# Optimization experiments

Measured on AMD Instinct MI355X. Metric: run time of the kernel, lower is better.

## Reference

```python
import jax, jax.numpy as jnp
import numpy as np
from jax import lax

INPUT_SIZE = 64          # classifier ROI size (init kwarg)
IMG = 640                # source image H=W
PROV, ALPHA, AD = 38, 25, 35
CONF_THRES, IOU_THRES = 0.25, 0.45
MAX_DET = 300            # yolov5 NMS max detections
FLAT = 16 * (INPUT_SIZE // 2) ** 2  # 16384


def setup_inputs() -> dict:
    key = jax.random.key(0)
    ks = jax.random.split(key, 12)
    B, N = 1, 25200
    xy = jax.random.uniform(ks[0], (B, N, 2), minval=32.0, maxval=608.0)
    wh = jax.random.uniform(ks[1], (B, N, 2), minval=16.0, maxval=128.0)
    obj = jax.random.uniform(ks[2], (B, N, 1))
    cls = jax.random.uniform(ks[3], (B, N, 1))
    preds = jnp.concatenate([xy, wh, obj, cls], axis=-1)  # [1,N,6] xywh+obj+cls
    image = jax.random.normal(ks[4], (B, 3, IMG, IMG), dtype=jnp.float32)
    W_conv = 0.1 * jax.random.normal(ks[5], (16, 3, 3, 3), dtype=jnp.float32)
    b_conv = jnp.zeros((16,), jnp.float32)
    W1 = 0.01 * jax.random.normal(ks[6], (8, FLAT, 128), dtype=jnp.float32)
    b1 = jnp.zeros((8, 128), jnp.float32)
    W2p = 0.05 * jax.random.normal(ks[7], (128, PROV), dtype=jnp.float32)
    b2p = jnp.zeros((PROV,), jnp.float32)
    W2a = 0.05 * jax.random.normal(ks[8], (128, ALPHA), dtype=jnp.float32)
    b2a = jnp.zeros((ALPHA,), jnp.float32)
    W2d = 0.05 * jax.random.normal(ks[9], (6, 128, AD), dtype=jnp.float32)
    b2d = jnp.zeros((6, AD), jnp.float32)
    return {"preds": preds, "image": image, "W_conv": W_conv, "b_conv": b_conv,
            "W1": W1, "b1": b1, "W2p": W2p, "b2p": b2p, "W2a": W2a, "b2a": b2a,
            "W2d": W2d, "b2d": b2d}


def _pairwise_iou(b):
    # b: [K,4] xyxy
    x1, y1, x2, y2 = b[:, 0], b[:, 1], b[:, 2], b[:, 3]
    area = (x2 - x1) * (y2 - y1)
    iw = jnp.clip(jnp.minimum(x2[:, None], x2[None, :]) - jnp.maximum(x1[:, None], x1[None, :]), 0.0)
    ih = jnp.clip(jnp.minimum(y2[:, None], y2[None, :]) - jnp.maximum(y1[:, None], y1[None, :]), 0.0)
    inter = iw * ih
    return inter / (area[:, None] + area[None, :] - inter + 1e-7)


def reference(preds, image, W_conv, b_conv, W1, b1, W2p, b2p, W2a, b2a, W2d, b2d):
    # ---- NMS (yolov5-style, single class) ----
    p = preds[0]                                   # [N,6]
    score = p[:, 4] * p[:, 5]                      # obj_conf * cls_conf
    xy, wh = p[:, 0:2], p[:, 2:4]
    boxes = jnp.concatenate([xy - wh / 2, xy + wh / 2], axis=-1)  # xyxy
    masked = jnp.where(score > CONF_THRES, score, -jnp.inf)
    top_s, idx = lax.top_k(masked, MAX_DET)        # sorted desc
    b = boxes[idx]                                 # [K,4]
    valid = top_s > CONF_THRES
    ious = _pairwise_iou(b)                        # [K,K]
    ar = jnp.arange(MAX_DET)

    def body(i, keep):
        sup = jnp.any((ious[i] > IOU_THRES) & keep & (ar < i))
        return keep.at[i].set(keep[i] & jnp.logical_not(sup))

    keep = lax.fori_loop(0, MAX_DET, body, valid)  # greedy suppression

    # ---- fixed-size ROI crop at box top-left (clipped) ----
    x1 = jnp.clip(jnp.round(b[:, 0]).astype(jnp.int32), 0, IMG - INPUT_SIZE)
    y1 = jnp.clip(jnp.round(b[:, 1]).astype(jnp.int32), 0, IMG - INPUT_SIZE)
    img0 = image[0]                                # [3,H,W]
    crops = jax.vmap(lambda y, x: lax.dynamic_slice(img0, (0, y, x), (3, INPUT_SIZE, INPUT_SIZE)))(y1, x1)

    # ---- LicensePlateClassifier: conv->relu->maxpool->flatten->8 heads ----
    conv = lax.conv_general_dilated(crops, W_conv, (1, 1), 'SAME',
                                    dimension_numbers=('NCHW', 'OIHW', 'NCHW'))
    conv = jax.nn.relu(conv + b_conv[None, :, None, None])
    pooled = lax.reduce_window(conv, -jnp.inf, lax.max, (1, 1, 2, 2), (1, 1, 2, 2), 'VALID')
    feats = pooled.reshape(MAX_DET, FLAT)          # NCHW flatten == torch.flatten(x,1)
    h = jax.nn.relu(jnp.einsum('kf,hfd->hkd', feats, W1) + b1[:, None, :])  # [8,K,128]
    out_p = h[0] @ W2p + b2p                       # [K,38]
    out_a = h[1] @ W2a + b2a                       # [K,25]
    out_d = jnp.einsum('hkd,hdo->hko', h[2:], W2d) + b2d[:, None, :]        # [6,K,35]
    out_d = out_d.transpose(1, 0, 2).reshape(MAX_DET, 6 * AD)
    logits = jnp.concatenate([out_p, out_a, out_d], axis=1)  # [K,273]
    return logits * keep.astype(logits.dtype)[:, None]
```

## Files before the change

kernel.cpp:

```cpp
#include <hip/hip_runtime.h>

#define N_PRED 25200
#define CONF 0.25f
#define IOU_THR 0.45f
#define MAXD 300
#define IMGW 640
#define CROPW 64
#define HISTN 16640
#define KSPLIT 16

typedef float f32x4 __attribute__((ext_vector_type(4)));
typedef short s16x8 __attribute__((ext_vector_type(8)));
typedef unsigned long long u64;

#define OFF_HIST   0u
#define OFF_CNT    66560u
#define OFF_CAND   66816u
#define CTRL_BYTES 75008u
#define OFF_BOXES  75008u
#define OFF_XY1    79872u
#define OFF_VALID  82432u
#define OFF_KEEP   83712u
#define OFF_SUP    84992u
#define OFF_FEATS  1325824u
#define OFF_PART   11811584u

__device__ inline unsigned short f2bf(float x) {
  unsigned u = __float_as_uint(x);
  u += 0x7FFFu + ((u >> 16) & 1u);
  return (unsigned short)(u >> 16);
}

__global__ __launch_bounds__(256) void k_hist(const float* __restrict__ preds,
                                              unsigned* __restrict__ hist) {
  int i = blockIdx.x * 256 + threadIdx.x;
  if (i >= N_PRED) return;
  float s = preds[i * 6 + 4] * preds[i * 6 + 5];
  if (s > CONF) atomicAdd(&hist[__float_as_uint(s) >> 16], 1u);
}

__global__ __launch_bounds__(256) void k_compact(const float* __restrict__ preds,
                                                 const unsigned* __restrict__ hist,
                                                 unsigned* __restrict__ cnt,
                                                 u64* __restrict__ cand) {
  __shared__ unsigned s[256];
  __shared__ unsigned scut;
  int t = threadIdx.x;
  int base = t * 65;
  unsigned local = 0;
  for (int i = 0; i < 65; ++i) local += hist[base + i];
  s[t] = local;
  __syncthreads();
  for (int off = 1; off < 256; off <<= 1) {
    unsigned add = (t + off < 256) ? s[t + off] : 0u;
    __syncthreads();
    s[t] += add;
    __syncthreads();
  }
  unsigned incl = s[t];
  unsigned excl = (t < 255) ? s[t + 1] : 0u;
  if (t == 0) scut = 0u;
  __syncthreads();
  if (incl >= (unsigned)MAXD && excl < (unsigned)MAXD) {
    unsigned acc = excl, res = 0u;
    #pragma unroll
    for (int ii = 64; ii >= 0; --ii) {
      acc += hist[base + ii];
      if (res == 0u && acc >= (unsigned)MAXD) res = (unsigned)(base + ii);
    }
    scut = res;
  }
  __syncthreads();
  unsigned cutv = scut;

  int i = blockIdx.x * 256 + t;
  if (i >= N_PRED) return;
  float sc = preds[i * 6 + 4] * preds[i * 6 + 5];
  if (sc <= CONF) return;
  unsigned bits = __float_as_uint(sc);
  if ((bits >> 16) < cutv) return;
  unsigned pos = atomicAdd(cnt, 1u);
  if (pos < 1024u)
    cand[pos] = ((u64)bits << 32) | (u64)(0xFFFFFFFFu - (unsigned)i);
}

__global__ __launch_bounds__(1024) void k_sortprep(const float* __restrict__ preds,
                                                   const u64* __restrict__ cand,
                                                   float* __restrict__ boxes,
                                                   int* __restrict__ xy1,
                                                   float* __restrict__ validf) {
  __shared__ u64 sk[1024];
  int t = threadIdx.x;
  sk[t] = cand[t];
  __syncthreads();
  for (int k = 2; k <= 1024; k <<= 1)
    for (int j = k >> 1; j > 0; j >>= 1) {
      int p = t ^ j;
      if (p > t) {
        u64 a = sk[t], b = sk[p];
        bool up = ((t & k) == 0);
        bool sw = up ? (a < b) : (a > b);
        if (sw) { sk[t] = b; sk[p] = a; }
      }
      __syncthreads();
    }
  if (t < MAXD) {
    u64 key = sk[t];
    if (key != 0ull) {
      int idx = (int)(0xFFFFFFFFu - (unsigned)(key & 0xFFFFFFFFull));
      float cx = preds[idx * 6 + 0], cy = preds[idx * 6 + 1];
      float w  = preds[idx * 6 + 2], h  = preds[idx * 6 + 3];
      float x1 = cx - w * 0.5f, y1 = cy - h * 0.5f;
      float x2 = cx + w * 0.5f, y2 = cy + h * 0.5f;
      boxes[t * 4 + 0] = x1; boxes[t * 4 + 1] = y1;
      boxes[t * 4 + 2] = x2; boxes[t * 4 + 3] = y2;
      int xi = (int)rintf(x1); xi = min(max(xi, 0), IMGW - CROPW);
      int yi = (int)rintf(y1); yi = min(max(yi, 0), IMGW - CROPW);
      xy1[t * 2 + 0] = xi; xy1[t * 2 + 1] = yi;
      validf[t] = 1.0f;
    } else {
      boxes[t * 4 + 0] = 0.f; boxes[t * 4 + 1] = 0.f;
      boxes[t * 4 + 2] = 0.f; boxes[t * 4 + 3] = 0.f;
      xy1[t * 2 + 0] = 0; xy1[t * 2 + 1] = 0;
      validf[t] = 0.f;
    }
  }
}

__global__ __launch_bounds__(320) void k_iou(const float* __restrict__ boxes,
                                             u64* __restrict__ sup) {
  int i = blockIdx.x, t = threadIdx.x;
  int w = t >> 6, lane = t & 63;
  f32x4 bi = *(const f32x4*)&boxes[i * 4];
  f32x4 bj = (t < MAXD) ? *(const f32x4*)&boxes[t * 4]
                        : (f32x4){0.f, 0.f, 0.f, 0.f};
  float ar  = (bi[2] - bi[0]) * (bi[3] - bi[1]);
  float arj = (bj[2] - bj[0]) * (bj[3] - bj[1]);
  float iw = fmaxf(fminf(bi[2], bj[2]) - fmaxf(bi[0], bj[0]), 0.f);
  float ih = fmaxf(fminf(bi[3], bj[3]) - fmaxf(bi[1], bj[1]), 0.f);
  float inter = iw * ih;
  float iou = inter / (ar + arj - inter + 1e-7f);
  u64 bm = __ballot((t < MAXD) && (iou > IOU_THR));
  if (lane == 0) sup[i * 5 + w] = bm;
}

__global__ __launch_bounds__(64) void k_nms(const u64* __restrict__ sup,
                                            const float* __restrict__ validf,
                                            float* __restrict__ keepf) {
  int lane = threadIdx.x;
  u64 srow[5][5];
  #pragma unroll
  for (int c = 0; c < 5; ++c)
    #pragma unroll
    for (int ww = 0; ww < 5; ++ww) srow[c][ww] = 0ull;
  #pragma unroll
  for (int c = 0; c < 5; ++c) {
    int i = c * 64 + lane;
    if (i < MAXD) {
      #pragma unroll
      for (int ww = 0; ww <= c; ++ww) srow[c][ww] = sup[i * 5 + ww];
    }
  }
  u64 validm[5];
  #pragma unroll
  for (int c = 0; c < 5; ++c) {
    int i = c * 64 + lane;
    float vf = (i < MAXD) ? validf[i] : 0.f;
    validm[c] = __ballot(vf > 0.5f);
  }
  u64 kw0 = 0, kw1 = 0, kw2 = 0, kw3 = 0;
  #pragma unroll
  for (int c = 0; c < 5; ++c) {
    bool ext = ((srow[c][0] & kw0) | (srow[c][1] & kw1) |
                (srow[c][2] & kw2) | (srow[c][3] & kw3)) != 0ull;
    u64 alive = validm[c] & __ballot(!ext);
    unsigned mlo = (unsigned)srow[c][c], mhi = (unsigned)(srow[c][c] >> 32);
    u64 rem = alive;
    while (rem) {
      int b = (int)__builtin_ctzll(rem);
      u64 gt = (b == 63) ? 0ull : (~0ull << (b + 1));
      u64 mi = ((u64)(unsigned)__builtin_amdgcn_readlane((int)mhi, b) << 32) |
               (u64)(unsigned)__builtin_amdgcn_readlane((int)mlo, b);
      alive &= ~(mi & gt);
      rem = alive & gt;
    }
    int i = c * 64 + lane;
    if (i < MAXD) keepf[i] = ((alive >> lane) & 1ull) ? 1.f : 0.f;
    if (c == 0) kw0 = alive;
    else if (c == 1) kw1 = alive;
    else if (c == 2) kw2 = alive;
    else if (c == 3) kw3 = alive;
  }
}

__global__ __launch_bounds__(256) void k_cropconv(const float* __restrict__ image,
                                                  const float* __restrict__ Wc,
                                                  const float* __restrict__ bc,
                                                  const int* __restrict__ xy1,
                                                  short* __restrict__ feats) {
  __shared__ __align__(16) float crop[3][10][68];
  int det = blockIdx.x, sl = blockIdx.y, tid = threadIdx.x;
  int pr0 = sl * 4;
  int gyBase = pr0 * 2 - 1;
  int ch = tid >> 4, px = tid & 15;

  float w[27];
  #pragma unroll
  for (int i = 0; i < 27; i++) w[i] = Wc[ch * 27 + i];
  float bias = bc[ch];

  int x0 = xy1[det * 2 + 0], y0 = xy1[det * 2 + 1];
  float sv[8];
  #pragma unroll
  for (int i = 0; i < 8; i++) {
    int u = tid + i * 256;
    float v = 0.f;
    if (u < 1920) {
      int row = u >> 6, x = u & 63;
      int c = row / 10, ry = row - c * 10;
      int gy = gyBase + ry;
      if (gy >= 0 && gy < CROPW)
        v = image[(size_t)c * (IMGW * IMGW) + (y0 + gy) * IMGW + x0 + x];
    }
    sv[i] = v;
  }
  if (tid < 120) {
    int row = tid >> 2, e = tid & 3;
    int c = row / 10, ry = row - c * 10;
    crop[c][ry][(e == 0) ? 0 : (64 + e)] = 0.f;
  }
  #pragma unroll
  for (int i = 0; i < 8; i++) {
    int u = tid + i * 256;
    if (u < 1920) {
      int row = u >> 6, x = u & 63;
      int c = row / 10, ry = row - c * 10;
      crop[c][ry][x + 1] = sv[i];
    }
  }
  __syncthreads();
  #pragma unroll
  for (int pr = 0; pr < 4; pr++) {
    float acc0[4] = {0.f, 0.f, 0.f, 0.f};
    float acc1[4] = {0.f, 0.f, 0.f, 0.f};
    #pragma unroll
    for (int c = 0; c < 3; c++) {
      #pragma unroll
      for (int r = 0; r < 4; r++) {
        const float* rp = &crop[c][2 * pr + r][4 * px];
        f32x4 v4 = *(const f32x4*)rp;
        float2 v2 = *(const float2*)(rp + 4);
        float in[6] = {v4[0], v4[1], v4[2], v4[3], v2.x, v2.y};
        if (r <= 2) {
          const float w0 = w[c * 9 + r * 3], w1 = w[c * 9 + r * 3 + 1],
                      w2 = w[c * 9 + r * 3 + 2];
          #pragma unroll
          for (int q = 0; q < 4; q++)
            acc0[q] += in[q] * w0 + in[q + 1] * w1 + in[q + 2] * w2;
        }
        if (r >= 1) {
          const float w0 = w[c * 9 + (r - 1) * 3], w1 = w[c * 9 + (r - 1) * 3 + 1],
                      w2 = w[c * 9 + (r - 1) * 3 + 2];
          #pragma unroll
          for (int q = 0; q < 4; q++)
            acc1[q] += in[q] * w0 + in[q + 1] * w1 + in[q + 2] * w2;
        }
      }
    }
    float m0 = fmaxf(fmaxf(acc0[0], acc0[1]), fmaxf(acc1[0], acc1[1]));
    float m1 = fmaxf(fmaxf(acc0[2], acc0[3]), fmaxf(acc1[2], acc1[3]));
    unsigned lo = f2bf(fmaxf(m0 + bias, 0.f));
    unsigned hi = f2bf(fmaxf(m1 + bias, 0.f));
    *(unsigned*)&feats[(size_t)det * 16384 + ch * 1024 + (pr0 + pr) * 32 + 2 * px] =
        lo | (hi << 16);
  }
}

__global__ __launch_bounds__(512, 2) void k_gemm(const short* __restrict__ feats,
                                                 const float* __restrict__ W1,
                                                 float* __restrict__ part) {
  __shared__ __align__(16) short As[2][320 * 64];
  int tid = threadIdx.x;
  int wid = tid >> 6, lane = tid & 63;
  int wm = wid & 3, wn = wid >> 2;
  int lr = lane & 15, kg = lane >> 4;
  int ks = blockIdx.x, hd = blockIdx.y, dh = blockIdx.z;
  const int f0 = ks * 1024, d0 = dh * 64;
  const float* w1h = W1 + (size_t)hd * 16384 * 128;

  f32x4 acc[5][2];
  #pragma unroll
  for (int i = 0; i < 5; i++)
    #pragma unroll
    for (int j = 0; j < 2; j++) acc[i][j] = (f32x4){0.f, 0.f, 0.f, 0.f};

  s16x8 aR[5];
  #pragma unroll
  for (int i = 0; i < 5; i++) {
    int ch = tid + i * 512, m = ch >> 3, c = ch & 7;
    aR[i] = *(const s16x8*)(feats + (size_t)m * 16384 + f0 + c * 8);
  }
  const float* bp = w1h + (size_t)(f0 + kg * 8) * 128 + d0 + wn * 32 + lr;
  float bF[2][2][8];
  #pragma unroll
  for (int k32 = 0; k32 < 2; k32++)
    #pragma unroll
    for (int nf = 0; nf < 2; nf++)
      #pragma unroll
      for (int j = 0; j < 8; j++)
        bF[k32][nf][j] = bp[(k32 * 32 + j) * 128 + nf * 16];
  #pragma unroll
  for (int i = 0; i < 5; i++) {
    int ch = tid + i * 512, m = ch >> 3, c = ch & 7;
    *(s16x8*)((char*)&As[0][0] + m * 128 + ((c ^ (m & 7)) << 4)) = aR[i];
  }
  __syncthreads();

  for (int t = 0; t < 16; ++t) {
    int cur = t & 1;
    s16x8 bfr[2][2];
    #pragma unroll
    for (int k32 = 0; k32 < 2; k32++)
      #pragma unroll
      for (int nf = 0; nf < 2; nf++)
        #pragma unroll
        for (int j = 0; j < 8; j++)
          bfr[k32][nf][j] = (short)f2bf(bF[k32][nf][j]);
    bool pf = (t + 1) < 16;
    if (pf) {
      int f1 = f0 + (t + 1) * 64;
      #pragma unroll
      for (int i = 0; i < 5; i++) {
        int ch = tid + i * 512, m = ch >> 3, c = ch & 7;
        aR[i] = *(const s16x8*)(feats + (size_t)m * 16384 + f1 + c * 8);
      }
      const float* bp2 = bp + (size_t)(t + 1) * 64 * 128;
      #pragma unroll
      for (int k32 = 0; k32 < 2; k32++)
        #pragma unroll
        for (int nf = 0; nf < 2; nf++)
          #pragma unroll
          for (int j = 0; j < 8; j++)
            bF[k32][nf][j] = bp2[(k32 * 32 + j) * 128 + nf * 16];
    }
    #pragma unroll
    for (int k32 = 0; k32 < 2; ++k32) {
      s16x8 af[5];
      #pragma unroll
      for (int mf = 0; mf < 5; ++mf) {
        int row = wm * 80 + mf * 16 + lr;
        int c = k32 * 4 + kg;
        af[mf] = *(const s16x8*)((const char*)&As[cur][0] + row * 128 + ((c ^ (row & 7)) << 4));
      }
      #pragma unroll
      for (int nf = 0; nf < 2; ++nf)
        #pragma unroll
        for (int mf = 0; mf < 5; ++mf)
          acc[mf][nf] = __builtin_amdgcn_mfma_f32_16x16x32_bf16(af[mf], bfr[k32][nf], acc[mf][nf], 0, 0, 0);
    }
    if (pf) {
      #pragma unroll
      for (int i = 0; i < 5; i++) {
        int ch = tid + i * 512, m = ch >> 3, c = ch & 7;
        *(s16x8*)((char*)&As[cur ^ 1][0] + m * 128 + ((c ^ (m & 7)) << 4)) = aR[i];
      }
      __syncthreads();
    }
  }
  #pragma unroll
  for (int mf = 0; mf < 5; ++mf)
    #pragma unroll
    for (int nf = 0; nf < 2; ++nf)
      #pragma unroll
      for (int r = 0; r < 4; ++r) {
        int m = wm * 80 + mf * 16 + kg * 4 + r;
        int d = d0 + wn * 32 + nf * 16 + lr;
        part[(((size_t)ks * 8 + hd) * 320 + m) * 128 + d] = acc[mf][nf][r];
      }
}

__global__ __launch_bounds__(320) void k_fc2(const float* __restrict__ part,
                                             const float* __restrict__ b1,
                                             const float* __restrict__ keepf,
                                             const float* __restrict__ W2p,
                                             const float* __restrict__ b2p,
                                             const float* __restrict__ W2a,
                                             const float* __restrict__ b2a,
                                             const float* __restrict__ W2d,
                                             const float* __restrict__ b2d,
                                             float* __restrict__ out) {
  int det = blockIdx.x, t = threadIdx.x;
  __shared__ float hl[1024];
  for (int i = t; i < 1024; i += 320) {
    int hh = i >> 7, d = i & 127;
    float s = 0.f;
    #pragma unroll
    for (int ksp = 0; ksp < KSPLIT; ksp++)
      s += part[(((size_t)ksp * 8 + hh) * 320 + det) * 128 + d];
    hl[i] = fmaxf(s + b1[hh * 128 + d], 0.f);
  }
  __syncthreads();
  if (t >= 273) return;
  float kf = keepf[det];
  float s = 0.f, bias;
  if (t < 38) {
    const float* hp = hl;
    for (int d = 0; d < 128; d++) s += hp[d] * W2p[d * 38 + t];
    bias = b2p[t];
  } else if (t < 63) {
    int c = t - 38;
    const float* hp = hl + 128;
    for (int d = 0; d < 128; d++) s += hp[d] * W2a[d * 25 + c];
    bias = b2a[c];
  } else {
    int u = t - 63, j = u / 35, o = u - j * 35;
    const float* hp = hl + (2 + j) * 128;
    for (int d = 0; d < 128; d++) s += hp[d] * W2d[((size_t)j * 128 + d) * 35 + o];
    bias = b2d[j * 35 + o];
  }
  out[det * 273 + t] = (s + bias) * kf;
}

extern "C" void kernel_launch(void* const* d_in, const int* in_sizes, int n_in,
                              void* d_out, int out_size, void* d_ws, size_t ws_size,
                              hipStream_t stream) {
  (void)in_sizes; (void)n_in; (void)out_size; (void)ws_size;
  const float* preds = (const float*)d_in[0];
  const float* image = (const float*)d_in[1];
  const float* Wc    = (const float*)d_in[2];
  const float* bc    = (const float*)d_in[3];
  const float* W1    = (const float*)d_in[4];
  const float* b1    = (const float*)d_in[5];
  const float* W2p   = (const float*)d_in[6];
  const float* b2p   = (const float*)d_in[7];
  const float* W2a   = (const float*)d_in[8];
  const float* b2a   = (const float*)d_in[9];
  const float* W2d   = (const float*)d_in[10];
  const float* b2d   = (const float*)d_in[11];

  char* ws = (char*)d_ws;
  unsigned* hist   = (unsigned*)(ws + OFF_HIST);
  unsigned* cnt    = (unsigned*)(ws + OFF_CNT);
  u64*      cand   = (u64*)(ws + OFF_CAND);
  float*    boxes  = (float*)(ws + OFF_BOXES);
  int*      xy1    = (int*)(ws + OFF_XY1);
  float*    validf = (float*)(ws + OFF_VALID);
  float*    keepf  = (float*)(ws + OFF_KEEP);
  u64*      sup    = (u64*)(ws + OFF_SUP);
  short*    feats  = (short*)(ws + OFF_FEATS);
  float*    part   = (float*)(ws + OFF_PART);
  float*    out    = (float*)d_out;

  hipMemsetAsync(ws, 0, CTRL_BYTES, stream);
  k_hist<<<(N_PRED + 255) / 256, 256, 0, stream>>>(preds, hist);
  k_compact<<<(N_PRED + 255) / 256, 256, 0, stream>>>(preds, hist, cnt, cand);
  k_sortprep<<<1, 1024, 0, stream>>>(preds, cand, boxes, xy1, validf);
  k_iou<<<MAXD, 320, 0, stream>>>(boxes, sup);
  k_nms<<<1, 64, 0, stream>>>(sup, validf, keepf);
  k_cropconv<<<dim3(300, 8), 256, 0, stream>>>(image, Wc, bc, xy1, feats);
  k_gemm<<<dim3(KSPLIT, 8, 2), 512, 0, stream>>>(feats, W1, part);
  k_fc2<<<MAXD, 320, 0, stream>>>(part, b1, keepf, W2p, b2p, W2a, b2a, W2d, b2d, out);
}
```

Measured before the change: 119.9 us.

## Fuse sort, IoU matrix and NMS into a single-block select kernel

Merges the sort/box-prep, pairwise IoU bitmask, and greedy NMS kernels into one 1024-thread kernel. Boxes, suppression masks and validity stay in shared memory instead of going through global workspace. This removes two kernel launches and their global round-trips. In exchange, the IoU matrix is computed by a single block of 16 waves rather than 300 blocks, which serializes that work.

```diff
diff --git a/kernel.cpp b/kernel.cpp
--- a/kernel.cpp
+++ b/kernel.cpp
@@ -17,11 +17,8 @@
 #define OFF_CNT    66560u
 #define OFF_CAND   66816u
 #define CTRL_BYTES 75008u
-#define OFF_BOXES  75008u
 #define OFF_XY1    79872u
-#define OFF_VALID  82432u
 #define OFF_KEEP   83712u
-#define OFF_SUP    84992u
 #define OFF_FEATS  1325824u
 #define OFF_PART   11811584u
 
@@ -84,13 +81,16 @@
     cand[pos] = ((u64)bits << 32) | (u64)(0xFFFFFFFFu - (unsigned)i);
 }
 
-__global__ __launch_bounds__(1024) void k_sortprep(const float* __restrict__ preds,
-                                                   const u64* __restrict__ cand,
-                                                   float* __restrict__ boxes,
-                                                   int* __restrict__ xy1,
-                                                   float* __restrict__ validf) {
+__global__ __launch_bounds__(1024) void k_select(const float* __restrict__ preds,
+                                                 const u64* __restrict__ cand,
+                                                 int* __restrict__ xy1,
+                                                 float* __restrict__ keepf) {
   __shared__ u64 sk[1024];
+  __shared__ __align__(16) float sb[MAXD * 4];
+  __shared__ u64 ssup[MAXD * 5];
+  __shared__ float svalid[MAXD];
   int t = threadIdx.x;
+
   sk[t] = cand[t];
   __syncthreads();
   for (int k = 2; k <= 1024; k <<= 1)
@@ -104,6 +104,7 @@
       }
       __syncthreads();
     }
+
   if (t < MAXD) {
     u64 key = sk[t];
     if (key != 0ull) {
@@ -112,84 +113,93 @@
       float w  = preds[idx * 6 + 2], h  = preds[idx * 6 + 3];
       float x1 = cx - w * 0.5f, y1 = cy - h * 0.5f;
       float x2 = cx + w * 0.5f, y2 = cy + h * 0.5f;
-      boxes[t * 4 + 0] = x1; boxes[t * 4 + 1] = y1;
-      boxes[t * 4 + 2] = x2; boxes[t * 4 + 3] = y2;
+      sb[t * 4 + 0] = x1; sb[t * 4 + 1] = y1;
+      sb[t * 4 + 2] = x2; sb[t * 4 + 3] = y2;
       int xi = (int)rintf(x1); xi = min(max(xi, 0), IMGW - CROPW);
       int yi = (int)rintf(y1); yi = min(max(yi, 0), IMGW - CROPW);
       xy1[t * 2 + 0] = xi; xy1[t * 2 + 1] = yi;
-      validf[t] = 1.0f;
+      svalid[t] = 1.0f;
     } else {
-      boxes[t * 4 + 0] = 0.f; boxes[t * 4 + 1] = 0.f;
-      boxes[t * 4 + 2] = 0.f; boxes[t * 4 + 3] = 0.f;
+      sb[t * 4 + 0] = 0.f; sb[t * 4 + 1] = 0.f;
+      sb[t * 4 + 2] = 0.f; sb[t * 4 + 3] = 0.f;
       xy1[t * 2 + 0] = 0; xy1[t * 2 + 1] = 0;
-      validf[t] = 0.f;
-    }
-  }
-}
-
-__global__ __launch_bounds__(320) void k_iou(const float* __restrict__ boxes,
-                                             u64* __restrict__ sup) {
-  int i = blockIdx.x, t = threadIdx.x;
-  int w = t >> 6, lane = t & 63;
-  f32x4 bi = *(const f32x4*)&boxes[i * 4];
-  f32x4 bj = (t < MAXD) ? *(const f32x4*)&boxes[t * 4]
-                        : (f32x4){0.f, 0.f, 0.f, 0.f};
-  float ar  = (bi[2] - bi[0]) * (bi[3] - bi[1]);
-  float arj = (bj[2] - bj[0]) * (bj[3] - bj[1]);
-  float iw = fmaxf(fminf(bi[2], bj[2]) - fmaxf(bi[0], bj[0]), 0.f);
-  float ih = fmaxf(fminf(bi[3], bj[3]) - fmaxf(bi[1], bj[1]), 0.f);
-  float inter = iw * ih;
-  float iou = inter / (ar + arj - inter + 1e-7f);
-  u64 bm = __ballot((t < MAXD) && (iou > IOU_THR));
-  if (lane == 0) sup[i * 5 + w] = bm;
-}
-
-__global__ __launch_bounds__(64) void k_nms(const u64* __restrict__ sup,
-                                            const float* __restrict__ validf,
-                                            float* __restrict__ keepf) {
-  int lane = threadIdx.x;
-  u64 srow[5][5];
-  #pragma unroll
-  for (int c = 0; c < 5; ++c)
-    #pragma unroll
-    for (int ww = 0; ww < 5; ++ww) srow[c][ww] = 0ull;
-  #pragma unroll
-  for (int c = 0; c < 5; ++c) {
-    int i = c * 64 + lane;
-    if (i < MAXD) {
-      #pragma unroll
-      for (int ww = 0; ww <= c; ++ww) srow[c][ww] = sup[i * 5 + ww];
-    }
-  }
-  u64 validm[5];
-  #pragma unroll
-  for (int c = 0; c < 5; ++c) {
-    int i = c * 64 + lane;
-    float vf = (i < MAXD) ? validf[i] : 0.f;
-    validm[c] = __ballot(vf > 0.5f);
-  }
-  u64 kw0 = 0, kw1 = 0, kw2 = 0, kw3 = 0;
-  #pragma unroll
-  for (int c = 0; c < 5; ++c) {
-    bool ext = ((srow[c][0] & kw0) | (srow[c][1] & kw1) |
-                (srow[c][2] & kw2) | (srow[c][3] & kw3)) != 0ull;
-    u64 alive = validm[c] & __ballot(!ext);
-    unsigned mlo = (unsigned)srow[c][c], mhi = (unsigned)(srow[c][c] >> 32);
-    u64 rem = alive;
-    while (rem) {
-      int b = (int)__builtin_ctzll(rem);
-      u64 gt = (b == 63) ? 0ull : (~0ull << (b + 1));
-      u64 mi = ((u64)(unsigned)__builtin_amdgcn_readlane((int)mhi, b) << 32) |
-               (u64)(unsigned)__builtin_amdgcn_readlane((int)mlo, b);
-      alive &= ~(mi & gt);
-      rem = alive & gt;
-    }
-    int i = c * 64 + lane;
-    if (i < MAXD) keepf[i] = ((alive >> lane) & 1ull) ? 1.f : 0.f;
-    if (c == 0) kw0 = alive;
-    else if (c == 1) kw1 = alive;
-    else if (c == 2) kw2 = alive;
-    else if (c == 3) kw3 = alive;
+      svalid[t] = 0.f;
+    }
+  }
+  __syncthreads();
+
+  {
+    int w = t >> 6, lane = t & 63;
+    f32x4 bj[5]; float arj[5];
+    #pragma unroll
+    for (int cc = 0; cc < 5; ++cc) {
+      int col = cc * 64 + lane;
+      bj[cc] = (col < MAXD) ? *(const f32x4*)&sb[col * 4]
+                            : (f32x4){0.f, 0.f, 0.f, 0.f};
+      arj[cc] = (bj[cc][2] - bj[cc][0]) * (bj[cc][3] - bj[cc][1]);
+    }
+    for (int row = w; row < MAXD; row += 16) {
+      f32x4 bi = *(const f32x4*)&sb[row * 4];
+      float ar = (bi[2] - bi[0]) * (bi[3] - bi[1]);
+      #pragma unroll
+      for (int cc = 0; cc < 5; ++cc) {
+        int col = cc * 64 + lane;
+        float iw = fmaxf(fminf(bi[2], bj[cc][2]) - fmaxf(bi[0], bj[cc][0]), 0.f);
+        float ih = fmaxf(fminf(bi[3], bj[cc][3]) - fmaxf(bi[1], bj[cc][1]), 0.f);
+        float inter = iw * ih;
+        float iou = inter / (ar + arj[cc] - inter + 1e-7f);
+        u64 bm = __ballot((col < MAXD) && (iou > IOU_THR));
+        if (lane == 0) ssup[row * 5 + cc] = bm;
+      }
+    }
+  }
+  __syncthreads();
+
+  if (t < 64) {
+    int lane = t;
+    u64 srow[5][5];
+    #pragma unroll
+    for (int c = 0; c < 5; ++c)
+      #pragma unroll
+      for (int ww = 0; ww < 5; ++ww) srow[c][ww] = 0ull;
+    #pragma unroll
+    for (int c = 0; c < 5; ++c) {
+      int i = c * 64 + lane;
+      if (i < MAXD) {
+        #pragma unroll
+        for (int ww = 0; ww <= c; ++ww) srow[c][ww] = ssup[i * 5 + ww];
+      }
+    }
+    u64 validm[5];
+    #pragma unroll
+    for (int c = 0; c < 5; ++c) {
+      int i = c * 64 + lane;
+      float vf = (i < MAXD) ? svalid[i] : 0.f;
+      validm[c] = __ballot(vf > 0.5f);
+    }
+    u64 kw0 = 0, kw1 = 0, kw2 = 0, kw3 = 0;
+    #pragma unroll
+    for (int c = 0; c < 5; ++c) {
+      bool ext = ((srow[c][0] & kw0) | (srow[c][1] & kw1) |
+                  (srow[c][2] & kw2) | (srow[c][3] & kw3)) != 0ull;
+      u64 alive = validm[c] & __ballot(!ext);
+      unsigned mlo = (unsigned)srow[c][c], mhi = (unsigned)(srow[c][c] >> 32);
+      u64 rem = alive;
+      while (rem) {
+        int b = (int)__builtin_ctzll(rem);
+        u64 gt = (b == 63) ? 0ull : (~0ull << (b + 1));
+        u64 mi = ((u64)(unsigned)__builtin_amdgcn_readlane((int)mhi, b) << 32) |
+                 (u64)(unsigned)__builtin_amdgcn_readlane((int)mlo, b);
+        alive &= ~(mi & gt);
+        rem = alive & gt;
+      }
+      int i = c * 64 + lane;
+      if (i < MAXD) keepf[i] = ((alive >> lane) & 1ull) ? 1.f : 0.f;
+      if (c == 0) kw0 = alive;
+      else if (c == 1) kw1 = alive;
+      else if (c == 2) kw2 = alive;
+      else if (c == 3) kw3 = alive;
+    }
   }
 }
 
@@ -442,11 +452,8 @@
   unsigned* hist   = (unsigned*)(ws + OFF_HIST);
   unsigned* cnt    = (unsigned*)(ws + OFF_CNT);
   u64*      cand   = (u64*)(ws + OFF_CAND);
-  float*    boxes  = (float*)(ws + OFF_BOXES);
   int*      xy1    = (int*)(ws + OFF_XY1);
-  float*    validf = (float*)(ws + OFF_VALID);
   float*    keepf  = (float*)(ws + OFF_KEEP);
-  u64*      sup    = (u64*)(ws + OFF_SUP);
   short*    feats  = (short*)(ws + OFF_FEATS);
   float*    part   = (float*)(ws + OFF_PART);
   float*    out    = (float*)d_out;
@@ -454,9 +461,7 @@
   hipMemsetAsync(ws, 0, CTRL_BYTES, stream);
   k_hist<<<(N_PRED + 255) / 256, 256, 0, stream>>>(preds, hist);
   k_compact<<<(N_PRED + 255) / 256, 256, 0, stream>>>(preds, hist, cnt, cand);
-  k_sortprep<<<1, 1024, 0, stream>>>(preds, cand, boxes, xy1, validf);
-  k_iou<<<MAXD, 320, 0, stream>>>(boxes, sup);
-  k_nms<<<1, 64, 0, stream>>>(sup, validf, keepf);
+  k_select<<<1, 1024, 0, stream>>>(preds, cand, xy1, keepf);
   k_cropconv<<<dim3(300, 8), 256, 0, stream>>>(image, Wc, bc, xy1, feats);
   k_gemm<<<dim3(KSPLIT, 8, 2), 512, 0, stream>>>(feats, W1, part);
   k_fc2<<<MAXD, 320, 0, stream>>>(part, b1, keepf, W2p, b2p, W2a, b2a, W2d, b2d, out);
```

After: 130.8 us. +9.1%, slower.
